# Performance work log

Measured on AMD Instinct MI355X. Metric: run time of the kernel, lower is better.

Reference implementation:

```python
import math
import jax, jax.numpy as jnp
import numpy as np

B, S, D = 4, 2048, 1024
NEG = -1e20

def setup_inputs() -> dict:
    key = jax.random.key(0)
    k1, k2, k3, k4 = jax.random.split(key, 4)
    X = jax.random.normal(k1, (B, S, D), dtype=jnp.float32)
    # True = masked position (masked_fill semantics)
    attention_mask = jax.random.randint(k2, (B, S, S), 0, 2).astype(bool)
    scale = 1.0 / math.sqrt(D)
    W_qkv = jax.random.normal(k3, (D, 3 * D), dtype=jnp.float32) * scale
    b_qkv = jnp.zeros((3 * D,), dtype=jnp.float32)
    W_out = jax.random.normal(k4, (D, D), dtype=jnp.float32) * scale
    b_out = jnp.zeros((D,), dtype=jnp.float32)
    return {"X": X, "attention_mask": attention_mask,
            "W_qkv": W_qkv, "b_qkv": b_qkv, "W_out": W_out, "b_out": b_out}

def reference(X, attention_mask, W_qkv, b_qkv, W_out, b_out):
    dim = X.shape[-1]
    QKV = X @ W_qkv + b_qkv                      # [B,S,3D]
    Q, K, V = jnp.split(QKV, 3, axis=-1)         # each [B,S,D]
    scores = jnp.einsum('bqd,bkd->bqk', Q, K) / math.sqrt(dim)  # [B,S,S]
    scores = jnp.where(attention_mask, NEG, scores)
    attn = jax.nn.softmax(scores, axis=-1)       # dropout_rate=0.0 -> identity
    ctx = jnp.einsum('bqk,bkd->bqd', attn, V)    # [B,S,D]
    return ctx @ W_out + b_out
```

## Files before the change

kernel.cpp:

```cpp
#include <hip/hip_runtime.h>
#include <cstdint>
#include <cstddef>

#define BB 4
#define SS 2048
#define DD 1024

typedef _Float16 f16;
typedef _Float16 f16x8 __attribute__((ext_vector_type(8)));
typedef _Float16 f16x4 __attribute__((ext_vector_type(4)));
typedef float fx4 __attribute__((ext_vector_type(4)));

__device__ __forceinline__ void async_copy16(void* lds, const void* g) {
  __builtin_amdgcn_global_load_lds(
      (__attribute__((address_space(1))) void*)const_cast<void*>(g),
      (__attribute__((address_space(3))) void*)lds,
      16, 0, 0);
}

enum { EPI_BIAS = 0, EPI_MASKEXP = 1, EPI_ROWSCALE = 2, EPI_QKV = 3 };

template <typename OutT, int MODE>
__global__ __launch_bounds__(256, 2) void gemm_nt(
    const f16* __restrict__ A, long long strideA, int lda,
    const f16* __restrict__ Bt, long long strideB, int ldb,
    OutT* __restrict__ C, long long strideC, int ldc,
    const float* __restrict__ bias, const int* __restrict__ mask,
    float* __restrict__ rowSum, f16* __restrict__ vt, float scale, int K) {
  constexpr int SMEM_BYTES = (MODE == EPI_MASKEXP) ? 34816 : 32768;
  __shared__ __align__(16) char smem[SMEM_BYTES];
  uint32_t* lmb = (uint32_t*)(smem + 32768);

  const int t = threadIdx.x;
  const int lane = t & 63;
  const int wid = t >> 6;
  const long long bz = blockIdx.z;

  const int nxy = gridDim.x * gridDim.y;
  const int bxy = blockIdx.y * gridDim.x + blockIdx.x;
  const int chunk = nxy >> 3;
  const int wk = (bxy & 7) * chunk + (bxy >> 3);
  const int tileN = (wk % gridDim.x) * 128;
  const int tileM = (wk / gridDim.x) * 128;

  const f16* Ab = A + bz * strideA;
  const f16* Bb = Bt + bz * strideB;
  OutT* Cb = C + bz * strideC;

  const int sr = t >> 2;
  const int sc = (((t & 3) ^ ((t >> 3) & 3)) * 8);
  const f16* pa0 = Ab + (size_t)(tileM + sr) * lda + sc;
  const f16* pa1 = Ab + (size_t)(tileM + 64 + sr) * lda + sc;
  const f16* pb0 = Bb + (size_t)(tileN + sr) * ldb + sc;
  const f16* pb1 = Bb + (size_t)(tileN + 64 + sr) * ldb + sc;
  const int tb = t * 16;

  const int waveM = (wid >> 1) * 64;
  const int waveN = (wid & 1) * 64;
  const int r16 = lane & 15;
  const int quad = lane >> 4;
  const int sw = (r16 >> 1) & 3;

  if constexpr (MODE == EPI_MASKEXP) {
    const int* maskb = mask + bz * (long long)SS * SS;
#pragma unroll
    for (int it = 0; it < 16; ++it) {
      const int f = it * 256 + t;
      const int4 mv =
          *(const int4*)&maskb[(size_t)(tileM + (f >> 5)) * SS + tileN + (f & 31) * 4];
      uint32_t val = (mv.x ? 1u : 0u) | (mv.y ? 2u : 0u) | (mv.z ? 4u : 0u) |
                     (mv.w ? 8u : 0u);
      val <<= (t & 7) * 4;
      val |= __shfl_xor(val, 1, 64);
      val |= __shfl_xor(val, 2, 64);
      val |= __shfl_xor(val, 4, 64);
      if ((t & 7) == 0) lmb[it * 32 + (t >> 3)] = val;
    }
    __syncthreads();
  }

  const int nIter = K >> 5;
  {
    char* b0 = smem;
    async_copy16(b0 + tb, pa0);
    async_copy16(b0 + 4096 + tb, pa1);
    async_copy16(b0 + 8192 + tb, pb0);
    async_copy16(b0 + 12288 + tb, pb1);
  }

  fx4 acc[4][4] = {};

#pragma unroll 2
  for (int i = 0; i < nIter; ++i) {
    __syncthreads();
    if (i + 1 < nIter) {
      char* nb = smem + ((i + 1) & 1) * 16384;
      const int k = (i + 1) << 5;
      async_copy16(nb + tb, pa0 + k);
      async_copy16(nb + 4096 + tb, pa1 + k);
      async_copy16(nb + 8192 + tb, pb0 + k);
      async_copy16(nb + 12288 + tb, pb1 + k);
    }
    const f16* As = (const f16*)(smem + (i & 1) * 16384);
    const f16* Bs = As + 4096;

    f16x8 af[4], bf[4];
#pragma unroll
    for (int x = 0; x < 4; ++x)
      af[x] = *(const f16x8*)&As[(waveM + x * 16 + r16) * 32 + (quad ^ sw) * 8];
#pragma unroll
    for (int x = 0; x < 4; ++x)
      bf[x] = *(const f16x8*)&Bs[(waveN + x * 16 + r16) * 32 + (quad ^ sw) * 8];

#pragma unroll
    for (int x = 0; x < 4; ++x)
#pragma unroll
      for (int j = 0; j < 4; ++j)
        acc[x][j] =
            __builtin_amdgcn_mfma_f32_16x16x32_f16(af[x], bf[j], acc[x][j], 0, 0, 0);
  }

  if constexpr (MODE == EPI_BIAS) {
#pragma unroll
    for (int j = 0; j < 4; ++j) {
      const int col = tileN + waveN + j * 16 + r16;
      const float bv = bias[col];
#pragma unroll
      for (int i = 0; i < 4; ++i) {
#pragma unroll
        for (int r = 0; r < 4; ++r) {
          const int row = tileM + waveM + i * 16 + quad * 4 + r;
          Cb[(size_t)row * ldc + col] = (OutT)(acc[i][j][r] * scale + bv);
        }
      }
    }
  } else if constexpr (MODE == EPI_QKV) {
    if (tileN < 2 * DD) {
#pragma unroll
      for (int j = 0; j < 4; ++j) {
        const int col = tileN + waveN + j * 16 + r16;
        const float bv = bias[col];
#pragma unroll
        for (int i = 0; i < 4; ++i) {
#pragma unroll
          for (int r = 0; r < 4; ++r) {
            const int row = tileM + waveM + i * 16 + quad * 4 + r;
            Cb[(size_t)row * ldc + col] = (OutT)(acc[i][j][r] + bv);
          }
        }
      }
    } else {
      const int b = tileM >> 11;
      const int s0 = (tileM & 2047) + waveM;
      f16* vb = vt + (size_t)b * DD * SS;
#pragma unroll
      for (int j = 0; j < 4; ++j) {
        const int col = tileN + waveN + j * 16 + r16;
        const float bv = bias[col];
        const int d = col - 2 * DD;
#pragma unroll
        for (int i = 0; i < 4; ++i) {
          const int s = s0 + i * 16 + quad * 4;
          f16x4 v4;
#pragma unroll
          for (int r = 0; r < 4; ++r) v4[r] = (f16)(acc[i][j][r] + bv);
          *(f16x4*)&vb[(size_t)d * SS + s] = v4;
        }
      }
    }
  } else if constexpr (MODE == EPI_MASKEXP) {
#pragma unroll
    for (int i = 0; i < 4; ++i) {
#pragma unroll
      for (int r = 0; r < 4; ++r) {
        const int lr = waveM + i * 16 + quad * 4 + r;
        const int row = tileM + lr;
        const uint32_t w0 = lmb[lr * 4 + (waveN >> 5)];
        const uint32_t w1 = lmb[lr * 4 + (waveN >> 5) + 1];
        float part = 0.0f;
#pragma unroll
        for (int j = 0; j < 4; ++j) {
          const int lc = waveN + j * 16 + r16;
          const int bitpos = j * 16 + r16;
          const uint32_t mv = ((j < 2 ? w0 : w1) >> (bitpos & 31)) & 1u;
          const float e = mv ? 0.0f : __expf(acc[i][j][r] * scale);
          Cb[(size_t)row * ldc + tileN + lc] = (OutT)e;
          part += e;
        }
#pragma unroll
        for (int d = 1; d < 16; d <<= 1) part += __shfl_xor(part, d, 64);
        if (r16 == 0) atomicAdd(&rowSum[bz * SS + row], part);
      }
    }
  } else {
#pragma unroll
    for (int i = 0; i < 4; ++i) {
#pragma unroll
      for (int r = 0; r < 4; ++r) {
        const int row = tileM + waveM + i * 16 + quad * 4 + r;
        const float inv = scale / rowSum[bz * SS + row];
#pragma unroll
        for (int j = 0; j < 4; ++j) {
          const int col = tileN + waveN + j * 16 + r16;
          Cb[(size_t)row * ldc + col] = (OutT)(acc[i][j][r] * inv);
        }
      }
    }
  }
}

__global__ __launch_bounds__(256) void k_prep(
    const float* __restrict__ X, f16* __restrict__ Xh,
    const float* __restrict__ Wqkv, f16* __restrict__ Wqkvt,
    const float* __restrict__ Wout, f16* __restrict__ Woutt,
    float* __restrict__ rowSum) {
  int bid = blockIdx.x;
  const int t = threadIdx.x;
  if (bid < 8192) {
    const int i = bid * 256 + t;
    const float4 v = ((const float4*)X)[i];
    f16x4 h = {(f16)v.x, (f16)v.y, (f16)v.z, (f16)v.w};
    ((f16x4*)Xh)[i] = h;
    return;
  }
  bid -= 8192;
  __shared__ float tile[32][33];
  const int tx = t & 31, ty = t >> 5;
  if (bid < 3072) {
    const int bx = (bid % 96) * 32, by = (bid / 96) * 32;
    for (int i2 = ty; i2 < 32; i2 += 8)
      tile[i2][tx] = Wqkv[(size_t)(by + i2) * 3072 + bx + tx];
    __syncthreads();
    for (int i2 = ty; i2 < 32; i2 += 8)
      Wqkvt[(size_t)(bx + i2) * 1024 + by + tx] = (f16)tile[tx][i2];
    return;
  }
  bid -= 3072;
  if (bid < 1024) {
    const int bx = (bid & 31) * 32, by = (bid >> 5) * 32;
    for (int i2 = ty; i2 < 32; i2 += 8)
      tile[i2][tx] = Wout[(size_t)(by + i2) * 1024 + bx + tx];
    __syncthreads();
    for (int i2 = ty; i2 < 32; i2 += 8)
      Woutt[(size_t)(bx + i2) * 1024 + by + tx] = (f16)tile[tx][i2];
    return;
  }
  bid -= 1024;
  rowSum[bid * 256 + t] = 0.0f;
}

extern "C" void kernel_launch(void* const* d_in, const int* in_sizes, int n_in,
                              void* d_out, int out_size, void* d_ws, size_t ws_size,
                              hipStream_t stream) {
  const float* X = (const float*)d_in[0];
  const int* mask = (const int*)d_in[1];
  const float* Wqkv = (const float*)d_in[2];
  const float* bqkv = (const float*)d_in[3];
  const float* Wout = (const float*)d_in[4];
  const float* bout = (const float*)d_in[5];
  float* out = (float*)d_out;

  char* ws = (char*)d_ws;
  f16* Xh = (f16*)(ws + 0);
  f16* Wqkvt = (f16*)(ws + 16777216);
  f16* Woutt = (f16*)(ws + 23068672);
  f16* QK = (f16*)(ws + 25165824);
  f16* Vt = (f16*)(ws + 58720256);
  f16* E = (f16*)(ws + 75497472);
  f16* Ctx = (f16*)(ws + 109051904);
  float* rowSum = (float*)(ws + 125829120);

  k_prep<<<dim3(12320), dim3(256), 0, stream>>>(X, Xh, Wqkv, Wqkvt, Wout, Woutt,
                                                rowSum);

  gemm_nt<f16, EPI_QKV><<<dim3(24, 64, 1), dim3(256), 0, stream>>>(
      Xh, 0LL, DD, Wqkvt, 0LL, DD, QK, 0LL, 2 * DD, bqkv, nullptr, nullptr, Vt,
      1.0f, DD);

  gemm_nt<f16, EPI_MASKEXP><<<dim3(16, 16, 4), dim3(256), 0, stream>>>(
      QK, (long long)SS * 2 * DD, 2 * DD, QK + DD, (long long)SS * 2 * DD, 2 * DD,
      E, (long long)SS * SS, SS, nullptr, mask, rowSum, nullptr, 0.03125f, DD);

  gemm_nt<f16, EPI_ROWSCALE><<<dim3(8, 16, 4), dim3(256), 0, stream>>>(
      E, (long long)SS * SS, SS, Vt, (long long)DD * SS, SS, Ctx,
      (long long)SS * DD, DD, nullptr, nullptr, rowSum, nullptr, 1.0f, SS);

  gemm_nt<float, EPI_BIAS><<<dim3(8, 64, 1), dim3(256), 0, stream>>>(
      Ctx, 0LL, DD, Woutt, 0LL, DD, out, 0LL, DD, bout, nullptr, nullptr, nullptr,
      1.0f, DD);
}
```

Baseline: 336.9 us.

## Pack attention mask into bitmask during QKV GEMM epilogue

Moves the int32-to-bit mask packing out of the scores kernel prologue into the tail of the QKV projection GEMM. Each of the first 1024 QKV blocks packs a contiguous 64 KB mask chunk into a global bitmask stored in the Ctx workspace region. The scores kernel then reads the packed bits from global memory in its epilogue instead of loading mask data into LDS before its main loop. This takes the mask read off the critical path of the attention-score GEMM and frees 2 KB of LDS, at the cost of extra work in the QKV kernel and uncached global reads of mask words in the epilogue.

```diff
diff --git a/kernel.cpp b/kernel.cpp
--- a/kernel.cpp
+++ b/kernel.cpp
@@ -26,10 +26,9 @@
     const f16* __restrict__ Bt, long long strideB, int ldb,
     OutT* __restrict__ C, long long strideC, int ldc,
     const float* __restrict__ bias, const int* __restrict__ mask,
-    float* __restrict__ rowSum, f16* __restrict__ vt, float scale, int K) {
-  constexpr int SMEM_BYTES = (MODE == EPI_MASKEXP) ? 34816 : 32768;
-  __shared__ __align__(16) char smem[SMEM_BYTES];
-  uint32_t* lmb = (uint32_t*)(smem + 32768);
+    uint32_t* __restrict__ gmask, float* __restrict__ rowSum,
+    f16* __restrict__ vt, float scale, int K) {
+  __shared__ __align__(16) char smem[32768];
 
   const int t = threadIdx.x;
   const int lane = t & 63;
@@ -60,24 +59,6 @@
   const int r16 = lane & 15;
   const int quad = lane >> 4;
   const int sw = (r16 >> 1) & 3;
-
-  if constexpr (MODE == EPI_MASKEXP) {
-    const int* maskb = mask + bz * (long long)SS * SS;
-#pragma unroll
-    for (int it = 0; it < 16; ++it) {
-      const int f = it * 256 + t;
-      const int4 mv =
-          *(const int4*)&maskb[(size_t)(tileM + (f >> 5)) * SS + tileN + (f & 31) * 4];
-      uint32_t val = (mv.x ? 1u : 0u) | (mv.y ? 2u : 0u) | (mv.z ? 4u : 0u) |
-                     (mv.w ? 8u : 0u);
-      val <<= (t & 7) * 4;
-      val |= __shfl_xor(val, 1, 64);
-      val |= __shfl_xor(val, 2, 64);
-      val |= __shfl_xor(val, 4, 64);
-      if ((t & 7) == 0) lmb[it * 32 + (t >> 3)] = val;
-    }
-    __syncthreads();
-  }
 
   const int nIter = K >> 5;
   {
@@ -168,23 +149,37 @@
         }
       }
     }
+    if (bxy < 1024) {
+      const int4* ms = (const int4*)(mask + (size_t)bxy * 16384);
+      uint32_t* gw = gmask + (size_t)bxy * 512;
+#pragma unroll
+      for (int it = 0; it < 16; ++it) {
+        const int4 mv = ms[it * 256 + t];
+        uint32_t val = (mv.x ? 1u : 0u) | (mv.y ? 2u : 0u) | (mv.z ? 4u : 0u) |
+                       (mv.w ? 8u : 0u);
+        val <<= (t & 7) * 4;
+        val |= __shfl_xor(val, 1, 64);
+        val |= __shfl_xor(val, 2, 64);
+        val |= __shfl_xor(val, 4, 64);
+        if ((t & 7) == 0) gw[it * 32 + (t >> 3)] = val;
+      }
+    }
   } else if constexpr (MODE == EPI_MASKEXP) {
 #pragma unroll
     for (int i = 0; i < 4; ++i) {
 #pragma unroll
       for (int r = 0; r < 4; ++r) {
-        const int lr = waveM + i * 16 + quad * 4 + r;
-        const int row = tileM + lr;
-        const uint32_t w0 = lmb[lr * 4 + (waveN >> 5)];
-        const uint32_t w1 = lmb[lr * 4 + (waveN >> 5) + 1];
+        const int row = tileM + waveM + i * 16 + quad * 4 + r;
+        const uint32_t* gr =
+            gmask + (((size_t)bz * SS + row) << 6) + ((tileN + waveN) >> 5);
+        const uint32_t w0 = gr[0], w1 = gr[1];
         float part = 0.0f;
 #pragma unroll
         for (int j = 0; j < 4; ++j) {
-          const int lc = waveN + j * 16 + r16;
           const int bitpos = j * 16 + r16;
           const uint32_t mv = ((j < 2 ? w0 : w1) >> (bitpos & 31)) & 1u;
           const float e = mv ? 0.0f : __expf(acc[i][j][r] * scale);
-          Cb[(size_t)row * ldc + tileN + lc] = (OutT)e;
+          Cb[(size_t)row * ldc + tileN + waveN + j * 16 + r16] = (OutT)e;
           part += e;
         }
 #pragma unroll
@@ -269,23 +264,26 @@
   f16* E = (f16*)(ws + 75497472);
   f16* Ctx = (f16*)(ws + 109051904);
   float* rowSum = (float*)(ws + 125829120);
+  uint32_t* gmask = (uint32_t*)(ws + 109051904);
 
   k_prep<<<dim3(12320), dim3(256), 0, stream>>>(X, Xh, Wqkv, Wqkvt, Wout, Woutt,
                                                 rowSum);
 
   gemm_nt<f16, EPI_QKV><<<dim3(24, 64, 1), dim3(256), 0, stream>>>(
-      Xh, 0LL, DD, Wqkvt, 0LL, DD, QK, 0LL, 2 * DD, bqkv, nullptr, nullptr, Vt,
-      1.0f, DD);
+      Xh, 0LL, DD, Wqkvt, 0LL, DD, QK, 0LL, 2 * DD, bqkv, mask, gmask, nullptr,
+      Vt, 1.0f, DD);
 
   gemm_nt<f16, EPI_MASKEXP><<<dim3(16, 16, 4), dim3(256), 0, stream>>>(
       QK, (long long)SS * 2 * DD, 2 * DD, QK + DD, (long long)SS * 2 * DD, 2 * DD,
-      E, (long long)SS * SS, SS, nullptr, mask, rowSum, nullptr, 0.03125f, DD);
+      E, (long long)SS * SS, SS, nullptr, nullptr, gmask, rowSum, nullptr,
+      0.03125f, DD);
 
   gemm_nt<f16, EPI_ROWSCALE><<<dim3(8, 16, 4), dim3(256), 0, stream>>>(
       E, (long long)SS * SS, SS, Vt, (long long)DD * SS, SS, Ctx,
-      (long long)SS * DD, DD, nullptr, nullptr, rowSum, nullptr, 1.0f, SS);
+      (long long)SS * DD, DD, nullptr, nullptr, nullptr, rowSum, nullptr, 1.0f,
+      SS);
 
   gemm_nt<float, EPI_BIAS><<<dim3(8, 64, 1), dim3(256), 0, stream>>>(
-      Ctx, 0LL, DD, Woutt, 0LL, DD, out, 0LL, DD, bout, nullptr, nullptr, nullptr,
-      1.0f, DD);
-}
+      Ctx, 0LL, DD, Woutt, 0LL, DD, out, 0LL, DD, bout, nullptr, nullptr,
+      nullptr, nullptr, 1.0f, DD);
+}
```

Measured after the change: 359.3 us. 1.07x slower.
